# Kernel optimization log

Hardware: AMD Instinct MI355X
Metric: run time of the kernel (lower is better)

The kernel has to match this reference:

```python
import jax, jax.numpy as jnp
import numpy as np

N_WORDS, MAX_CHARS = 32768, 16
WORD_DIM, CHAR_DIM, HIDDEN = 256, 64, 256
VOCAB = 256


def setup_inputs() -> dict:
    key = jax.random.key(0)
    ks = jax.random.split(key, 10)
    char_indices = jax.random.randint(ks[0], (N_WORDS, MAX_CHARS), 0, VOCAB)
    char_lengths = jax.random.randint(ks[1], (N_WORDS,), 1, MAX_CHARS + 1)
    word_emb = jax.random.normal(ks[2], (N_WORDS, WORD_DIM), dtype=jnp.float32)
    s = 0.05
    E_char = jax.random.normal(ks[3], (VOCAB, CHAR_DIM), dtype=jnp.float32) * s
    W_ih = jax.random.normal(ks[4], (4 * HIDDEN, CHAR_DIM), dtype=jnp.float32) * s
    W_hh = jax.random.normal(ks[5], (4 * HIDDEN, HIDDEN), dtype=jnp.float32) * s
    b_ih = jax.random.normal(ks[6], (4 * HIDDEN,), dtype=jnp.float32) * s
    b_hh = jax.random.normal(ks[7], (4 * HIDDEN,), dtype=jnp.float32) * s
    W_lin = jax.random.normal(ks[8], (WORD_DIM, WORD_DIM + HIDDEN), dtype=jnp.float32) * s
    b_lin = jax.random.normal(ks[9], (WORD_DIM,), dtype=jnp.float32) * s
    return dict(char_indices=char_indices, char_lengths=char_lengths,
                word_emb=word_emb, E_char=E_char, W_ih=W_ih, W_hh=W_hh,
                b_ih=b_ih, b_hh=b_hh, W_lin=W_lin, b_lin=b_lin)


def _lstm_last_hidden(x, lengths, W_ih, W_hh, b_ih, b_hh):
    # x: [N, T, E]; returns final hidden h at position length-1 per row.
    N, T, _ = x.shape
    H = W_hh.shape[1]
    x_proj = jnp.einsum('nte,ge->ntg', x, W_ih) + (b_ih + b_hh)  # [N, T, 4H]
    x_proj = jnp.transpose(x_proj, (1, 0, 2))                    # time-major [T, N, 4H]

    def step(carry, inp):
        h, c = carry
        xg, t = inp
        gates = xg + h @ W_hh.T
        i, f, g, o = jnp.split(gates, 4, axis=-1)
        i, f, o = jax.nn.sigmoid(i), jax.nn.sigmoid(f), jax.nn.sigmoid(o)
        g = jnp.tanh(g)
        c_new = f * c + i * g
        h_new = o * jnp.tanh(c_new)
        mask = (t < lengths)[:, None]  # freeze state past each word's length
        h = jnp.where(mask, h_new, h)
        c = jnp.where(mask, c_new, c)
        return (h, c), None

    h0 = jnp.zeros((N, H), dtype=x.dtype)
    c0 = jnp.zeros((N, H), dtype=x.dtype)
    (h, _), _ = jax.lax.scan(step, (h0, c0), (x_proj, jnp.arange(T)))
    return h


def reference(char_indices, char_lengths, word_emb, E_char, W_ih, W_hh,
              b_ih, b_hh, W_lin, b_lin):
    char_embedded = E_char[char_indices]                        # [N, T, E]
    h = _lstm_last_hidden(char_embedded, char_lengths, W_ih, W_hh, b_ih, b_hh)
    combined = jnp.concatenate([word_emb, h], axis=-1)          # [N, WORD+H]
    return jax.nn.relu(combined @ W_lin.T + b_lin)              # [N, WORD]
```

## Files before the change

kernel.cpp:

```cpp
#include <hip/hip_runtime.h>


#define NW 32768

typedef __attribute__((ext_vector_type(8))) short short8;
typedef __attribute__((ext_vector_type(4))) float f32x4;
typedef __attribute__((ext_vector_type(4))) int i32x4;

#define MFMA16(a,b,c) __builtin_amdgcn_mfma_f32_16x16x32_bf16(a,b,c,0,0,0)
#define MFMAI8(a,b,c) __builtin_amdgcn_mfma_i32_16x16x32_i8(a,b,c,0,0,0)

#define O_ORDER 0
#define O_SLEN  131072
#define O_WPK   262144
#define O_USTP  589824
#define O_BIAS  593920
#define O_CHT   598016
#define O_WLIN  614400

__device__ inline unsigned short f2b(float f) {
  unsigned u = __builtin_bit_cast(unsigned, f);
  u = u + 0x7fffu + ((u >> 16) & 1u);
  return (unsigned short)(u >> 16);
}
__device__ inline float fsigm(float x) {
  float e = __builtin_amdgcn_exp2f(-1.44269504f * x);
  return __builtin_amdgcn_rcpf(1.0f + e);
}
__device__ inline float ftanh(float x) {
  float e = __builtin_amdgcn_exp2f(2.88539008f * x);
  return 1.0f - 2.0f * __builtin_amdgcn_rcpf(e + 1.0f);
}

__global__ void k_prep0(const float* __restrict__ wih, const float* __restrict__ whh,
                        const float* __restrict__ bih, const float* __restrict__ bhh,
                        const float* __restrict__ ech, unsigned char* __restrict__ ws) {
  int i = blockIdx.x * 256 + threadIdx.x;
  if (i < 1024) {
    float mx = 0.f;
    for (int k = 0; k < 64; ++k)  mx = fmaxf(mx, fabsf(wih[i * 64 + k]) * 0.25f);
    for (int k = 0; k < 256; ++k) mx = fmaxf(mx, fabsf(whh[i * 256 + k]));
    ((float*)(ws + O_USTP))[i] = mx / (127.f * 127.f);
    ((float*)(ws + O_BIAS))[i] = bih[i] + bhh[i];
    return;
  }
  int j = i - 1024;
  if (j < 16384) {
    float v = 508.f * ech[j];
    int q = (int)__builtin_rintf(v);
    q = q < -127 ? -127 : (q > 127 ? 127 : q);
    ((signed char*)(ws + O_CHT))[j] = (signed char)q;
  }
}

__global__ void k_prep1(const float* __restrict__ wih, const float* __restrict__ whh,
                        const float* __restrict__ wlin, unsigned char* __restrict__ ws) {
  int i = blockIdx.x * 256 + threadIdx.x;
  if (i < 327680) {
    int j = i & 7, lane = (i >> 3) & 63, t2 = i >> 9;
    int nt = t2 & 7, u2 = t2 >> 3;
    int kb = u2 % 10, w = u2 / 10;
    int n = (nt >> 1) * 256 + w * 32 + (nt & 1) * 16 + (lane & 15);
    int k = kb * 32 + (lane >> 4) * 8 + j;
    float v = (k < 64) ? wih[n * 64 + k] * 0.25f : whh[n * 256 + (k - 64)];
    float ustep = ((const float*)(ws + O_USTP))[n] * 127.f;
    float qf = (ustep > 0.f) ? v / ustep : 0.f;
    int q = (int)__builtin_rintf(qf);
    q = q < -127 ? -127 : (q > 127 ? 127 : q);
    ((signed char*)(ws + O_WPK))[i] = (signed char)q;
    return;
  }
  int i2 = i - 327680;
  if (i2 < 131072) {
    int j = i2 & 7, lane = (i2 >> 3) & 63, t3 = i2 >> 9;
    int kf = t3 & 15, nn = t3 >> 4;
    int n = (nn >> 2) * 64 + (nn & 3) * 16 + (lane & 15);
    int k = kf * 32 + (lane >> 4) * 8 + j;
    ((unsigned short*)(ws + O_WLIN))[i2] = f2b(wlin[n * 512 + k]);
  }
}

__global__ void k_sort(const int* __restrict__ lens, unsigned char* __restrict__ ws) {
  __shared__ unsigned hist[16], pos[16];
  int tid = threadIdx.x;
  if (tid < 16) hist[tid] = 0;
  __syncthreads();
  for (int w = tid; w < NW; w += 1024) {
    int l = lens[w]; l = l < 1 ? 1 : (l > 16 ? 16 : l);
    atomicAdd(&hist[l - 1], 1u);
  }
  __syncthreads();
  if (tid == 0) {
    unsigned acc = 0;
    for (int l = 0; l < 16; ++l) { pos[l] = acc; acc += hist[l]; }
  }
  __syncthreads();
  int* order = (int*)(ws + O_ORDER);
  int* slenp = (int*)(ws + O_SLEN);
  for (int w = tid; w < NW; w += 1024) {
    int l = lens[w]; l = l < 1 ? 1 : (l > 16 ? 16 : l);
    unsigned p = atomicAdd(&pos[l - 1], 1u);
    order[p] = w; slenp[p] = l;
  }
}

__global__ __launch_bounds__(512, 2) void k_main(
    const int* __restrict__ cidx, const float* __restrict__ wemb,
    const float* __restrict__ blin, float* __restrict__ outp,
    const unsigned char* __restrict__ ws) {
  extern __shared__ signed char smem[];
  signed char (*WL)[8][8][64][8] = (signed char (*)[8][8][64][8])smem;
  signed char (*Xb)[10][64][8] = (signed char (*)[10][64][8])(smem + 98304);
  signed char (*CT)[64] = (signed char (*)[64])(smem + 98304 + 20480);
  int (*CW)[16] = (int (*)[16])(smem + 98304 + 20480 + 16384);

  const int tid = threadIdx.x, b = blockIdx.x;
  const int w = tid >> 6, lane = tid & 63;
  const int q = lane >> 4, l15 = lane & 15;

  const int* order = (const int*)(ws + O_ORDER);
  const int* slen  = (const int*)(ws + O_SLEN);
  const signed char* wpk = (const signed char*)(ws + O_WPK);
  const float* upt = (const float*)(ws + O_USTP);
  const float* bsg = (const float*)(ws + O_BIAS);
  const unsigned short* wlin = (const unsigned short*)(ws + O_WLIN);

  {
    long* d = (long*)&CT[0][0];
    const long* s = (const long*)(ws + O_CHT);
    #pragma unroll
    for (int ii = 0; ii < 4; ++ii) d[tid + 512 * ii] = s[tid + 512 * ii];
  }
  long wreg[7][8];
  #pragma unroll
  for (int kb = 0; kb < 7; ++kb)
    #pragma unroll
    for (int nt = 0; nt < 8; ++nt)
      wreg[kb][nt] = *(const long*)(wpk + (((w * 10 + kb) * 8 + nt) * 64 + lane) * 8);
  #pragma unroll
  for (int c = 0; c < 24; ++c) {
    int kb = c >> 3, nt = c & 7;
    *(long*)&WL[kb][w][nt][lane][0] =
        *(const long*)(wpk + (((w * 10 + 7 + kb) * 8 + nt) * 64 + lane) * 8);
  }
  float uq[8], bq[8];
  #pragma unroll
  for (int nt = 0; nt < 8; ++nt) {
    int n = (nt >> 1) * 256 + w * 32 + (nt & 1) * 16 + l15;
    uq[nt] = upt[n]; bq[nt] = bsg[n];
  }
  const int mh = w >> 2, nw = w & 3;
  float blv[4];
  #pragma unroll
  for (int nt = 0; nt < 4; ++nt) blv[nt] = blin[nw * 64 + nt * 16 + l15];

  for (int sl = 0; sl < 2; ++sl) {
    const int s = sl ? (511 - b) : b;
    const int base = 64 * s;
    __syncthreads();

    {
      long* p = (long*)&Xb[0][0][0][0];
      #pragma unroll
      for (int ii = 0; ii < 4; ++ii) {
        int idx = tid + 512 * ii;
        int mt = idx >> 9, rem = idx & 511;
        p[mt * 640 + 128 + rem] = 0L;
      }
    }
    if (tid < 256) {
      int m = tid >> 2, part = tid & 3;
      int wid = order[base + m];
      *(i32x4*)&CW[m][part * 4] = *(const i32x4*)(cidx + wid * 16 + part * 4);
    }
    int tmax[4]; unsigned lenpk[4];
    #pragma unroll
    for (int mt = 0; mt < 4; ++mt) {
      int pbm = base + 16 * mt;
      tmax[mt] = slen[pbm + 15];
      unsigned l0 = (unsigned)slen[pbm + q * 4 + 0];
      unsigned l1 = (unsigned)slen[pbm + q * 4 + 1];
      unsigned l2 = (unsigned)slen[pbm + q * 4 + 2];
      unsigned l3 = (unsigned)slen[pbm + q * 4 + 3];
      lenpk[mt] = l0 | (l1 << 8) | (l2 << 16) | (l3 << 24);
    }
    const int Tm = tmax[3];
    __syncthreads();
    {
      int m = tid >> 3, c = tid & 7, kb = c >> 2, kq = c & 3;
      int ch = CW[m][0] & 255;
      *(long*)&Xb[m >> 4][kb][(m & 15) + 16 * kq][0] = *(const long*)&CT[ch][kb * 32 + kq * 8];
    }
    __syncthreads();

    float creg[4][2][4];
    #pragma unroll
    for (int mt = 0; mt < 4; ++mt)
      #pragma unroll
      for (int hs = 0; hs < 2; ++hs)
        #pragma unroll
        for (int r = 0; r < 4; ++r) creg[mt][hs][r] = 0.f;
    unsigned hpack[4][2];

    for (int t = 0; t < Tm; ++t) {
      bool actm[4];
      actm[0] = t < tmax[0]; actm[1] = t < tmax[1];
      actm[2] = t < tmax[2]; actm[3] = true;

      #pragma unroll
      for (int mt = 0; mt < 4; ++mt) {
        if (!actm[mt]) continue;
        i32x4 acc[8];
        #pragma unroll
        for (int nt = 0; nt < 8; ++nt) acc[nt] = (i32x4)0;
        #pragma unroll
        for (int kb = 0; kb < 7; ++kb) {
          long A = *(const long*)&Xb[mt][kb][lane][0];
          #pragma unroll
          for (int nt = 0; nt < 8; ++nt) acc[nt] = MFMAI8(A, wreg[kb][nt], acc[nt]);
        }
        #pragma unroll
        for (int kb = 7; kb < 10; ++kb) {
          long A = *(const long*)&Xb[mt][kb][lane][0];
          #pragma unroll
          for (int nt = 0; nt < 8; ++nt) {
            long Bv = *(const long*)&WL[kb - 7][w][nt][lane][0];
            acc[nt] = MFMAI8(A, Bv, acc[nt]);
          }
        }
        #pragma unroll
        for (int hs = 0; hs < 2; ++hs) {
          unsigned hp = 0;
          #pragma unroll
          for (int r = 0; r < 4; ++r) {
            float gi = (float)acc[0 + hs][r] * uq[0 + hs] + bq[0 + hs];
            float gf = (float)acc[2 + hs][r] * uq[2 + hs] + bq[2 + hs];
            float gg = (float)acc[4 + hs][r] * uq[4 + hs] + bq[4 + hs];
            float go = (float)acc[6 + hs][r] * uq[6 + hs] + bq[6 + hs];
            float si = fsigm(gi), sf = fsigm(gf);
            float sg = ftanh(gg), so = fsigm(go);
            float cold = creg[mt][hs][r];
            float cn = sf * cold + si * sg;
            float hn = so * ftanh(cn);
            int lene = (int)((lenpk[mt] >> (8 * r)) & 255u);
            creg[mt][hs][r] = (t < lene) ? cn : cold;
            int hq = (int)__builtin_rintf(127.f * hn);
            hq = hq < -127 ? -127 : (hq > 127 ? 127 : hq);
            hp |= ((unsigned)hq & 255u) << (8 * r);
          }
          hpack[mt][hs] = hp;
        }
      }
      __syncthreads();

      #pragma unroll
      for (int mt = 0; mt < 4; ++mt) {
        if (!actm[mt]) continue;
        #pragma unroll
        for (int hs = 0; hs < 2; ++hs) {
          int kqp = hs * 2 + (l15 >> 3);
          #pragma unroll
          for (int r = 0; r < 4; ++r) {
            int lene = (int)((lenpk[mt] >> (8 * r)) & 255u);
            if (t < lene)
              Xb[mt][2 + w][(q * 4 + r) + 16 * kqp][l15 & 7] =
                  (signed char)((hpack[mt][hs] >> (8 * r)) & 255u);
          }
        }
      }
      if (t + 1 < Tm) {
        int m = tid >> 3, c = tid & 7, kb = c >> 2, kq = c & 3;
        int ch = CW[m][t + 1] & 255;
        *(long*)&Xb[m >> 4][kb][(m & 15) + 16 * kq][0] = *(const long*)&CT[ch][kb * 32 + kq * 8];
      }
      __syncthreads();
    }

    int widA[2];
    #pragma unroll
    for (int mi = 0; mi < 2; ++mi) widA[mi] = order[base + (2 * mh + mi) * 16 + l15];
    f32x4 fac[2][4];
    #pragma unroll
    for (int mi = 0; mi < 2; ++mi)
      #pragma unroll
      for (int nt = 0; nt < 4; ++nt) fac[mi][nt] = 0.0f;

    #pragma unroll
    for (int kf = 0; kf < 16; ++kf) {
      short8 Bn[4];
      #pragma unroll
      for (int nt = 0; nt < 4; ++nt)
        Bn[nt] = ((const short8*)wlin)[((nw * 4 + nt) * 16 + kf) * 64 + lane];
      short8 Am[2];
      #pragma unroll
      for (int mi = 0; mi < 2; ++mi) {
        if (kf < 8) {
          const f32x4* pa = (const f32x4*)(wemb + widA[mi] * 256 + kf * 32 + q * 8);
          f32x4 f0 = pa[0], f1 = pa[1];
          short8 A;
          A[0] = (short)f2b(f0[0]); A[1] = (short)f2b(f0[1]);
          A[2] = (short)f2b(f0[2]); A[3] = (short)f2b(f0[3]);
          A[4] = (short)f2b(f1[0]); A[5] = (short)f2b(f1[1]);
          A[6] = (short)f2b(f1[2]); A[7] = (short)f2b(f1[3]);
          Am[mi] = A;
        } else {
          long ch = *(const long*)&Xb[2 * mh + mi][kf - 6][lane][0];
          short8 A;
          #pragma unroll
          for (int j = 0; j < 8; ++j) {
            int v = (int)(signed char)((ch >> (8 * j)) & 255);
            A[j] = (short)f2b((float)v * (1.f / 127.f));
          }
          Am[mi] = A;
        }
      }
      #pragma unroll
      for (int mi = 0; mi < 2; ++mi)
        #pragma unroll
        for (int nt = 0; nt < 4; ++nt)
          fac[mi][nt] = MFMA16(Am[mi], Bn[nt], fac[mi][nt]);
    }
    #pragma unroll
    for (int mi = 0; mi < 2; ++mi) {
      #pragma unroll
      for (int r = 0; r < 4; ++r) {
        int wid = order[base + (2 * mh + mi) * 16 + q * 4 + r];
        float* po = outp + wid * 256 + nw * 64 + l15;
        #pragma unroll
        for (int nt = 0; nt < 4; ++nt) {
          float v = fac[mi][nt][r] + blv[nt];
          po[nt * 16] = v > 0.f ? v : 0.f;
        }
      }
    }
  }
}

extern "C" void kernel_launch(void* const* d_in, const int* in_sizes, int n_in,
                              void* d_out, int out_size, void* d_ws, size_t ws_size,
                              hipStream_t stream) {
  const int*   cidx = (const int*)d_in[0];
  const int*   clen = (const int*)d_in[1];
  const float* wemb = (const float*)d_in[2];
  const float* ech  = (const float*)d_in[3];
  const float* wih  = (const float*)d_in[4];
  const float* whh  = (const float*)d_in[5];
  const float* bih  = (const float*)d_in[6];
  const float* bhh  = (const float*)d_in[7];
  const float* wlin = (const float*)d_in[8];
  const float* blin = (const float*)d_in[9];
  float* outp = (float*)d_out;
  unsigned char* ws = (unsigned char*)d_ws;

  k_prep0<<<68, 256, 0, stream>>>(wih, whh, bih, bhh, ech, ws);
  k_prep1<<<1792, 256, 0, stream>>>(wih, whh, wlin, ws);
  k_sort<<<1, 1024, 0, stream>>>(clen, ws);
  k_main<<<256, 512, 139264, stream>>>(cidx, wemb, blin, outp, ws);
}
```

Baseline: 449.7 us.

## Use 1024-thread LSTM blocks with 16x16x64 int8 MFMA and parallel sort

The main kernel moves from 512 to 1024 threads per block, so each wave owns 16 hidden units across all four gates. The recurrent weights now fit entirely in registers using the wider i8 MFMA (K=64), which removes the LDS-resident weight slice. Cell state moves from registers into shared memory. The single-block length sort becomes a per-block histogram in the prep kernel, a prefix pass, and an atomic scatter kernel. The new scatter order is nondeterministic within a length bucket, and the cell state now costs an LDS round trip every step.

```diff
diff --git a/kernel.cpp b/kernel.cpp
--- a/kernel.cpp
+++ b/kernel.cpp
@@ -7,8 +7,8 @@
 typedef __attribute__((ext_vector_type(4))) float f32x4;
 typedef __attribute__((ext_vector_type(4))) int i32x4;
 
-#define MFMA16(a,b,c) __builtin_amdgcn_mfma_f32_16x16x32_bf16(a,b,c,0,0,0)
-#define MFMAI8(a,b,c) __builtin_amdgcn_mfma_i32_16x16x32_i8(a,b,c,0,0,0)
+#define MFMA16(a,b,c)  __builtin_amdgcn_mfma_f32_16x16x32_bf16(a,b,c,0,0,0)
+#define MFMAI64(a,b,c) __builtin_amdgcn_mfma_i32_16x16x64_i8(a,b,c,0,0,0)
 
 #define O_ORDER 0
 #define O_SLEN  131072
@@ -17,6 +17,8 @@
 #define O_BIAS  593920
 #define O_CHT   598016
 #define O_WLIN  614400
+#define O_HP    876544
+#define O_POS   877568
 
 __device__ inline unsigned short f2b(float f) {
   unsigned u = __builtin_bit_cast(unsigned, f);
@@ -32,36 +34,55 @@
   return 1.0f - 2.0f * __builtin_amdgcn_rcpf(e + 1.0f);
 }
 
-__global__ void k_prep0(const float* __restrict__ wih, const float* __restrict__ whh,
+__global__ void k_prepA(const float* __restrict__ wih, const float* __restrict__ whh,
                         const float* __restrict__ bih, const float* __restrict__ bhh,
-                        const float* __restrict__ ech, unsigned char* __restrict__ ws) {
-  int i = blockIdx.x * 256 + threadIdx.x;
-  if (i < 1024) {
-    float mx = 0.f;
-    for (int k = 0; k < 64; ++k)  mx = fmaxf(mx, fabsf(wih[i * 64 + k]) * 0.25f);
-    for (int k = 0; k < 256; ++k) mx = fmaxf(mx, fabsf(whh[i * 256 + k]));
-    ((float*)(ws + O_USTP))[i] = mx / (127.f * 127.f);
-    ((float*)(ws + O_BIAS))[i] = bih[i] + bhh[i];
+                        const float* __restrict__ ech, const int* __restrict__ lens,
+                        unsigned char* __restrict__ ws) {
+  int b = blockIdx.x, tid = threadIdx.x;
+  if (b < 256) {
+    int n = b * 4 + (tid >> 6), lane = tid & 63;
+    float m = fabsf(wih[n * 64 + lane]) * 0.25f;
+    #pragma unroll
+    for (int c = 0; c < 4; ++c) m = fmaxf(m, fabsf(whh[n * 256 + c * 64 + lane]));
+    #pragma unroll
+    for (int off = 32; off; off >>= 1) m = fmaxf(m, __shfl_xor(m, off));
+    if (lane == 0) {
+      ((float*)(ws + O_USTP))[n] = m / 16129.f;
+      ((float*)(ws + O_BIAS))[n] = bih[n] + bhh[n];
+    }
     return;
   }
-  int j = i - 1024;
-  if (j < 16384) {
-    float v = 508.f * ech[j];
-    int q = (int)__builtin_rintf(v);
+  if (b < 320) {
+    int idx = (b - 256) * 256 + tid;
+    int q = (int)__builtin_rintf(508.f * ech[idx]);
     q = q < -127 ? -127 : (q > 127 ? 127 : q);
-    ((signed char*)(ws + O_CHT))[j] = (signed char)q;
-  }
-}
-
-__global__ void k_prep1(const float* __restrict__ wih, const float* __restrict__ whh,
+    ((signed char*)(ws + O_CHT))[idx] = (signed char)q;
+    return;
+  }
+  __shared__ unsigned hist[16];
+  int blk = b - 320;
+  if (tid < 16) hist[tid] = 0;
+  __syncthreads();
+  #pragma unroll
+  for (int i = 0; i < 8; ++i) {
+    int w = blk * 2048 + i * 256 + tid;
+    int l = lens[w]; l = l < 1 ? 1 : (l > 16 ? 16 : l);
+    atomicAdd(&hist[l - 1], 1u);
+  }
+  __syncthreads();
+  if (tid < 16) ((unsigned*)(ws + O_HP))[blk * 16 + tid] = hist[tid];
+}
+
+__global__ void k_prepB(const float* __restrict__ wih, const float* __restrict__ whh,
                         const float* __restrict__ wlin, unsigned char* __restrict__ ws) {
-  int i = blockIdx.x * 256 + threadIdx.x;
-  if (i < 327680) {
-    int j = i & 7, lane = (i >> 3) & 63, t2 = i >> 9;
-    int nt = t2 & 7, u2 = t2 >> 3;
-    int kb = u2 % 10, w = u2 / 10;
-    int n = (nt >> 1) * 256 + w * 32 + (nt & 1) * 16 + (lane & 15);
-    int k = kb * 32 + (lane >> 4) * 8 + j;
+  int b = blockIdx.x, tid = threadIdx.x;
+  int i = b * 256 + tid;
+  if (b < 1280) {
+    int j = i & 15, lane = (i >> 4) & 63, t = i >> 10;
+    int g = t & 3, u = t >> 2;
+    int kb = u % 5, w = u / 5;
+    int n = g * 256 + w * 16 + (lane & 15);
+    int k = kb * 64 + (lane >> 4) * 16 + j;
     float v = (k < 64) ? wih[n * 64 + k] * 0.25f : whh[n * 256 + (k - 64)];
     float ustep = ((const float*)(ws + O_USTP))[n] * 127.f;
     float qf = (ustep > 0.f) ? v / ustep : 0.f;
@@ -70,49 +91,48 @@
     ((signed char*)(ws + O_WPK))[i] = (signed char)q;
     return;
   }
-  int i2 = i - 327680;
-  if (i2 < 131072) {
+  if (b < 1792) {
+    int i2 = i - 327680;
     int j = i2 & 7, lane = (i2 >> 3) & 63, t3 = i2 >> 9;
     int kf = t3 & 15, nn = t3 >> 4;
     int n = (nn >> 2) * 64 + (nn & 3) * 16 + (lane & 15);
     int k = kf * 32 + (lane >> 4) * 8 + j;
     ((unsigned short*)(ws + O_WLIN))[i2] = f2b(wlin[n * 512 + k]);
-  }
-}
-
-__global__ void k_sort(const int* __restrict__ lens, unsigned char* __restrict__ ws) {
-  __shared__ unsigned hist[16], pos[16];
-  int tid = threadIdx.x;
-  if (tid < 16) hist[tid] = 0;
-  __syncthreads();
-  for (int w = tid; w < NW; w += 1024) {
-    int l = lens[w]; l = l < 1 ? 1 : (l > 16 ? 16 : l);
-    atomicAdd(&hist[l - 1], 1u);
-  }
-  __syncthreads();
+    return;
+  }
   if (tid == 0) {
+    const unsigned* hp = (const unsigned*)(ws + O_HP);
+    int* pos = (int*)(ws + O_POS);
     unsigned acc = 0;
-    for (int l = 0; l < 16; ++l) { pos[l] = acc; acc += hist[l]; }
-  }
-  __syncthreads();
-  int* order = (int*)(ws + O_ORDER);
-  int* slenp = (int*)(ws + O_SLEN);
-  for (int w = tid; w < NW; w += 1024) {
-    int l = lens[w]; l = l < 1 ? 1 : (l > 16 ? 16 : l);
-    unsigned p = atomicAdd(&pos[l - 1], 1u);
-    order[p] = w; slenp[p] = l;
-  }
-}
-
-__global__ __launch_bounds__(512, 2) void k_main(
+    for (int l = 0; l < 16; ++l) {
+      unsigned s = 0;
+      for (int blk = 0; blk < 16; ++blk) s += hp[blk * 16 + l];
+      pos[l] = (int)acc; acc += s;
+    }
+  }
+}
+
+__global__ void k_scatter(const int* __restrict__ lens, unsigned char* __restrict__ ws) {
+  int w = blockIdx.x * 256 + threadIdx.x;
+  int l = lens[w]; l = l < 1 ? 1 : (l > 16 ? 16 : l);
+  int p = atomicAdd((int*)(ws + O_POS) + (l - 1), 1);
+  ((int*)(ws + O_ORDER))[p] = w;
+  ((int*)(ws + O_SLEN))[p]  = l;
+}
+
+#define L_XB  65536
+#define L_CT  86016
+#define L_CW  102400
+
+__global__ __launch_bounds__(1024, 4) void k_main(
     const int* __restrict__ cidx, const float* __restrict__ wemb,
     const float* __restrict__ blin, float* __restrict__ outp,
     const unsigned char* __restrict__ ws) {
-  extern __shared__ signed char smem[];
-  signed char (*WL)[8][8][64][8] = (signed char (*)[8][8][64][8])smem;
-  signed char (*Xb)[10][64][8] = (signed char (*)[10][64][8])(smem + 98304);
-  signed char (*CT)[64] = (signed char (*)[64])(smem + 98304 + 20480);
-  int (*CW)[16] = (int (*)[16])(smem + 98304 + 20480 + 16384);
+  extern __shared__ unsigned char smem[];
+  float* CRG = (float*)smem;
+  signed char (*Xb)[5][64][16] = (signed char (*)[5][64][16])(smem + L_XB);
+  signed char (*CT)[64] = (signed char (*)[64])(smem + L_CT);
+  int (*CW)[16] = (int (*)[16])(smem + L_CW);
 
   const int tid = threadIdx.x, b = blockIdx.x;
   const int w = tid >> 6, lane = tid & 63;
@@ -121,35 +141,23 @@
   const int* order = (const int*)(ws + O_ORDER);
   const int* slen  = (const int*)(ws + O_SLEN);
   const signed char* wpk = (const signed char*)(ws + O_WPK);
-  const float* upt = (const float*)(ws + O_USTP);
-  const float* bsg = (const float*)(ws + O_BIAS);
   const unsigned short* wlin = (const unsigned short*)(ws + O_WLIN);
 
-  {
-    long* d = (long*)&CT[0][0];
-    const long* s = (const long*)(ws + O_CHT);
-    #pragma unroll
-    for (int ii = 0; ii < 4; ++ii) d[tid + 512 * ii] = s[tid + 512 * ii];
-  }
-  long wreg[7][8];
+  ((i32x4*)CT)[tid] = ((const i32x4*)(ws + O_CHT))[tid];
+  i32x4 wreg[5][4];
   #pragma unroll
-  for (int kb = 0; kb < 7; ++kb)
-    #pragma unroll
-    for (int nt = 0; nt < 8; ++nt)
-      wreg[kb][nt] = *(const long*)(wpk + (((w * 10 + kb) * 8 + nt) * 64 + lane) * 8);
+  for (int kb = 0; kb < 5; ++kb)
+    #pragma unroll
+    for (int g = 0; g < 4; ++g)
+      wreg[kb][g] = *(const i32x4*)(wpk + (((w * 5 + kb) * 4 + g) * 64 + lane) * 16);
+  float uq[4], bq[4];
   #pragma unroll
-  for (int c = 0; c < 24; ++c) {
-    int kb = c >> 3, nt = c & 7;
-    *(long*)&WL[kb][w][nt][lane][0] =
-        *(const long*)(wpk + (((w * 10 + 7 + kb) * 8 + nt) * 64 + lane) * 8);
-  }
-  float uq[8], bq[8];
-  #pragma unroll
-  for (int nt = 0; nt < 8; ++nt) {
-    int n = (nt >> 1) * 256 + w * 32 + (nt & 1) * 16 + l15;
-    uq[nt] = upt[n]; bq[nt] = bsg[n];
-  }
-  const int mh = w >> 2, nw = w & 3;
+  for (int g = 0; g < 4; ++g) {
+    int n = g * 256 + w * 16 + l15;
+    uq[g] = ((const float*)(ws + O_USTP))[n];
+    bq[g] = ((const float*)(ws + O_BIAS))[n];
+  }
+  const int mt0 = w >> 2, nw = w & 3;
   float blv[4];
   #pragma unroll
   for (int nt = 0; nt < 4; ++nt) blv[nt] = blin[nw * 64 + nt * 16 + l15];
@@ -159,15 +167,10 @@
     const int base = 64 * s;
     __syncthreads();
 
-    {
-      long* p = (long*)&Xb[0][0][0][0];
-      #pragma unroll
-      for (int ii = 0; ii < 4; ++ii) {
-        int idx = tid + 512 * ii;
-        int mt = idx >> 9, rem = idx & 511;
-        p[mt * 640 + 128 + rem] = 0L;
-      }
-    }
+    ((i32x4*)Xb)[tid] = (i32x4)0;
+    if (tid < 256) ((i32x4*)Xb)[1024 + tid] = (i32x4)0;
+    #pragma unroll
+    for (int i = 0; i < 4; ++i) ((i32x4*)CRG)[tid + 1024 * i] = (i32x4)0;
     if (tid < 256) {
       int m = tid >> 2, part = tid & 3;
       int wid = order[base + m];
@@ -186,21 +189,14 @@
     }
     const int Tm = tmax[3];
     __syncthreads();
-    {
-      int m = tid >> 3, c = tid & 7, kb = c >> 2, kq = c & 3;
+    if (tid < 256) {
+      int m = tid >> 2, c = tid & 3;
       int ch = CW[m][0] & 255;
-      *(long*)&Xb[m >> 4][kb][(m & 15) + 16 * kq][0] = *(const long*)&CT[ch][kb * 32 + kq * 8];
+      *(i32x4*)&Xb[m >> 4][0][(m & 15) + 16 * c][0] = *(const i32x4*)&CT[ch][c * 16];
     }
     __syncthreads();
 
-    float creg[4][2][4];
-    #pragma unroll
-    for (int mt = 0; mt < 4; ++mt)
-      #pragma unroll
-      for (int hs = 0; hs < 2; ++hs)
-        #pragma unroll
-        for (int r = 0; r < 4; ++r) creg[mt][hs][r] = 0.f;
-    unsigned hpack[4][2];
+    unsigned hpack[4];
 
     for (int t = 0; t < Tm; ++t) {
       bool actm[4];
@@ -210,46 +206,34 @@
       #pragma unroll
       for (int mt = 0; mt < 4; ++mt) {
         if (!actm[mt]) continue;
-        i32x4 acc[8];
-        #pragma unroll
-        for (int nt = 0; nt < 8; ++nt) acc[nt] = (i32x4)0;
-        #pragma unroll
-        for (int kb = 0; kb < 7; ++kb) {
-          long A = *(const long*)&Xb[mt][kb][lane][0];
+        i32x4 acc[4];
+        #pragma unroll
+        for (int g = 0; g < 4; ++g) acc[g] = (i32x4)0;
+        #pragma unroll
+        for (int kb = 0; kb < 5; ++kb) {
+          i32x4 A = *(const i32x4*)&Xb[mt][kb][lane][0];
           #pragma unroll
-          for (int nt = 0; nt < 8; ++nt) acc[nt] = MFMAI8(A, wreg[kb][nt], acc[nt]);
+          for (int g = 0; g < 4; ++g) acc[g] = MFMAI64(A, wreg[kb][g], acc[g]);
         }
-        #pragma unroll
-        for (int kb = 7; kb < 10; ++kb) {
-          long A = *(const long*)&Xb[mt][kb][lane][0];
-          #pragma unroll
-          for (int nt = 0; nt < 8; ++nt) {
-            long Bv = *(const long*)&WL[kb - 7][w][nt][lane][0];
-            acc[nt] = MFMAI8(A, Bv, acc[nt]);
-          }
+        unsigned hp = 0;
+        #pragma unroll
+        for (int r = 0; r < 4; ++r) {
+          float gi = (float)acc[0][r] * uq[0] + bq[0];
+          float gf = (float)acc[1][r] * uq[1] + bq[1];
+          float gg = (float)acc[2][r] * uq[2] + bq[2];
+          float go = (float)acc[3][r] * uq[3] + bq[3];
+          float si = fsigm(gi), sf = fsigm(gf);
+          float sg = ftanh(gg), so = fsigm(go);
+          float cold = CRG[(mt * 4 + r) * 1024 + tid];
+          float cn = sf * cold + si * sg;
+          float hn = so * ftanh(cn);
+          int lene = (int)((lenpk[mt] >> (8 * r)) & 255u);
+          CRG[(mt * 4 + r) * 1024 + tid] = (t < lene) ? cn : cold;
+          int hq = (int)__builtin_rintf(127.f * hn);
+          hq = hq < -127 ? -127 : (hq > 127 ? 127 : hq);
+          hp |= ((unsigned)hq & 255u) << (8 * r);
         }
-        #pragma unroll
-        for (int hs = 0; hs < 2; ++hs) {
-          unsigned hp = 0;
-          #pragma unroll
-          for (int r = 0; r < 4; ++r) {
-            float gi = (float)acc[0 + hs][r] * uq[0 + hs] + bq[0 + hs];
-            float gf = (float)acc[2 + hs][r] * uq[2 + hs] + bq[2 + hs];
-            float gg = (float)acc[4 + hs][r] * uq[4 + hs] + bq[4 + hs];
-            float go = (float)acc[6 + hs][r] * uq[6 + hs] + bq[6 + hs];
-            float si = fsigm(gi), sf = fsigm(gf);
-            float sg = ftanh(gg), so = fsigm(go);
-            float cold = creg[mt][hs][r];
-            float cn = sf * cold + si * sg;
-            float hn = so * ftanh(cn);
-            int lene = (int)((lenpk[mt] >> (8 * r)) & 255u);
-            creg[mt][hs][r] = (t < lene) ? cn : cold;
-            int hq = (int)__builtin_rintf(127.f * hn);
-            hq = hq < -127 ? -127 : (hq > 127 ? 127 : hq);
-            hp |= ((unsigned)hq & 255u) << (8 * r);
-          }
-          hpack[mt][hs] = hp;
-        }
+        hpack[mt] = hp;
       }
       __syncthreads();
 
@@ -257,33 +241,25 @@
       for (int mt = 0; mt < 4; ++mt) {
         if (!actm[mt]) continue;
         #pragma unroll
-        for (int hs = 0; hs < 2; ++hs) {
-          int kqp = hs * 2 + (l15 >> 3);
-          #pragma unroll
-          for (int r = 0; r < 4; ++r) {
-            int lene = (int)((lenpk[mt] >> (8 * r)) & 255u);
-            if (t < lene)
-              Xb[mt][2 + w][(q * 4 + r) + 16 * kqp][l15 & 7] =
-                  (signed char)((hpack[mt][hs] >> (8 * r)) & 255u);
-          }
+        for (int r = 0; r < 4; ++r) {
+          int lene = (int)((lenpk[mt] >> (8 * r)) & 255u);
+          if (t < lene)
+            Xb[mt][1 + (w >> 2)][(q * 4 + r) + 16 * (w & 3)][l15] =
+                (signed char)((hpack[mt] >> (8 * r)) & 255u);
         }
       }
-      if (t + 1 < Tm) {
-        int m = tid >> 3, c = tid & 7, kb = c >> 2, kq = c & 3;
+      if (t + 1 < Tm && tid < 256) {
+        int m = tid >> 2, c = tid & 3;
         int ch = CW[m][t + 1] & 255;
-        *(long*)&Xb[m >> 4][kb][(m & 15) + 16 * kq][0] = *(const long*)&CT[ch][kb * 32 + kq * 8];
+        *(i32x4*)&Xb[m >> 4][0][(m & 15) + 16 * c][0] = *(const i32x4*)&CT[ch][c * 16];
       }
       __syncthreads();
     }
 
-    int widA[2];
-    #pragma unroll
-    for (int mi = 0; mi < 2; ++mi) widA[mi] = order[base + (2 * mh + mi) * 16 + l15];
-    f32x4 fac[2][4];
-    #pragma unroll
-    for (int mi = 0; mi < 2; ++mi)
-      #pragma unroll
-      for (int nt = 0; nt < 4; ++nt) fac[mi][nt] = 0.0f;
+    int widA = order[base + mt0 * 16 + l15];
+    f32x4 fac[4];
+    #pragma unroll
+    for (int nt = 0; nt < 4; ++nt) fac[nt] = 0.0f;
 
     #pragma unroll
     for (int kf = 0; kf < 16; ++kf) {
@@ -291,46 +267,34 @@
       #pragma unroll
       for (int nt = 0; nt < 4; ++nt)
         Bn[nt] = ((const short8*)wlin)[((nw * 4 + nt) * 16 + kf) * 64 + lane];
-      short8 Am[2];
-      #pragma unroll
-      for (int mi = 0; mi < 2; ++mi) {
-        if (kf < 8) {
-          const f32x4* pa = (const f32x4*)(wemb + widA[mi] * 256 + kf * 32 + q * 8);
-          f32x4 f0 = pa[0], f1 = pa[1];
-          short8 A;
-          A[0] = (short)f2b(f0[0]); A[1] = (short)f2b(f0[1]);
-          A[2] = (short)f2b(f0[2]); A[3] = (short)f2b(f0[3]);
-          A[4] = (short)f2b(f1[0]); A[5] = (short)f2b(f1[1]);
-          A[6] = (short)f2b(f1[2]); A[7] = (short)f2b(f1[3]);
-          Am[mi] = A;
-        } else {
-          long ch = *(const long*)&Xb[2 * mh + mi][kf - 6][lane][0];
-          short8 A;
-          #pragma unroll
-          for (int j = 0; j < 8; ++j) {
-            int v = (int)(signed char)((ch >> (8 * j)) & 255);
-            A[j] = (short)f2b((float)v * (1.f / 127.f));
-          }
-          Am[mi] = A;
+      short8 Am;
+      if (kf < 8) {
+        const f32x4* pa = (const f32x4*)(wemb + widA * 256 + kf * 32 + q * 8);
+        f32x4 f0 = pa[0], f1 = pa[1];
+        Am[0] = (short)f2b(f0[0]); Am[1] = (short)f2b(f0[1]);
+        Am[2] = (short)f2b(f0[2]); Am[3] = (short)f2b(f0[3]);
+        Am[4] = (short)f2b(f1[0]); Am[5] = (short)f2b(f1[1]);
+        Am[6] = (short)f2b(f1[2]); Am[7] = (short)f2b(f1[3]);
+      } else {
+        int K0 = 64 + (kf - 8) * 32 + q * 8;
+        long ch = *(const long*)&Xb[mt0][K0 >> 6][l15 + 16 * ((K0 >> 4) & 3)][K0 & 15];
+        #pragma unroll
+        for (int j = 0; j < 8; ++j) {
+          int v = (int)(signed char)((ch >> (8 * j)) & 255);
+          Am[j] = (short)f2b((float)v * (1.f / 127.f));
         }
       }
       #pragma unroll
-      for (int mi = 0; mi < 2; ++mi)
-        #pragma unroll
-        for (int nt = 0; nt < 4; ++nt)
-          fac[mi][nt] = MFMA16(Am[mi], Bn[nt], fac[mi][nt]);
-    }
-    #pragma unroll
-    for (int mi = 0; mi < 2; ++mi) {
-      #pragma unroll
-      for (int r = 0; r < 4; ++r) {
-        int wid = order[base + (2 * mh + mi) * 16 + q * 4 + r];
-        float* po = outp + wid * 256 + nw * 64 + l15;
-        #pragma unroll
-        for (int nt = 0; nt < 4; ++nt) {
-          float v = fac[mi][nt][r] + blv[nt];
-          po[nt * 16] = v > 0.f ? v : 0.f;
-        }
+      for (int nt = 0; nt < 4; ++nt) fac[nt] = MFMA16(Am, Bn[nt], fac[nt]);
+    }
+    #pragma unroll
+    for (int r = 0; r < 4; ++r) {
+      int wid = order[base + mt0 * 16 + q * 4 + r];
+      float* po = outp + wid * 256 + nw * 64 + l15;
+      #pragma unroll
+      for (int nt = 0; nt < 4; ++nt) {
+        float v = fac[nt][r] + blv[nt];
+        po[nt * 16] = v > 0.f ? v : 0.f;
       }
     }
   }
@@ -352,8 +316,8 @@
   float* outp = (float*)d_out;
   unsigned char* ws = (unsigned char*)d_ws;
 
-  k_prep0<<<68, 256, 0, stream>>>(wih, whh, bih, bhh, ech, ws);
-  k_prep1<<<1792, 256, 0, stream>>>(wih, whh, wlin, ws);
-  k_sort<<<1, 1024, 0, stream>>>(clen, ws);
-  k_main<<<256, 512, 139264, stream>>>(cidx, wemb, blin, outp, ws);
-}
+  k_prepA<<<336, 256, 0, stream>>>(wih, whh, bih, bhh, ech, clen, ws);
+  k_prepB<<<1793, 256, 0, stream>>>(wih, whh, wlin, ws);
+  k_scatter<<<128, 256, 0, stream>>>(clen, ws);
+  k_main<<<256, 1024, 106496, stream>>>(cidx, wemb, blin, outp, ws);
+}
```

After: 571.3 us. +27.0%, slower.

## Merge gate reciprocals, drop per-tile time skipping, parallelize weight-scale prep

Applied to the files above, without the earlier changes.

The LSTM cell math now folds the sigmoid and tanh reciprocals into fewer rcp calls, so i*g and o*tanh(c) each use a single reciprocal of a product, with clamping added to avoid overflow. The per-16-row tile activity check is removed, so every tile runs the MFMA and gate work for all steps up to the block's maximum length. The state is still frozen through per-row length masks. The prep kernel computes per-row max-abs scales with a wave-wide shuffle reduction instead of a serial loop per thread. Removing the skip adds wasted work for short words in sorted blocks, in exchange for fewer transcendental ops and less branching.

```diff
diff --git a/kernel.cpp b/kernel.cpp
--- a/kernel.cpp
+++ b/kernel.cpp
@@ -23,34 +23,28 @@
   u = u + 0x7fffu + ((u >> 16) & 1u);
   return (unsigned short)(u >> 16);
 }
-__device__ inline float fsigm(float x) {
-  float e = __builtin_amdgcn_exp2f(-1.44269504f * x);
-  return __builtin_amdgcn_rcpf(1.0f + e);
-}
-__device__ inline float ftanh(float x) {
-  float e = __builtin_amdgcn_exp2f(2.88539008f * x);
-  return 1.0f - 2.0f * __builtin_amdgcn_rcpf(e + 1.0f);
-}
-
-__global__ void k_prep0(const float* __restrict__ wih, const float* __restrict__ whh,
+
+__global__ void k_prepA(const float* __restrict__ wih, const float* __restrict__ whh,
                         const float* __restrict__ bih, const float* __restrict__ bhh,
                         const float* __restrict__ ech, unsigned char* __restrict__ ws) {
-  int i = blockIdx.x * 256 + threadIdx.x;
-  if (i < 1024) {
-    float mx = 0.f;
-    for (int k = 0; k < 64; ++k)  mx = fmaxf(mx, fabsf(wih[i * 64 + k]) * 0.25f);
-    for (int k = 0; k < 256; ++k) mx = fmaxf(mx, fabsf(whh[i * 256 + k]));
-    ((float*)(ws + O_USTP))[i] = mx / (127.f * 127.f);
-    ((float*)(ws + O_BIAS))[i] = bih[i] + bhh[i];
+  int b = blockIdx.x, tid = threadIdx.x;
+  if (b < 256) {
+    int n = b * 4 + (tid >> 6), lane = tid & 63;
+    float m = fabsf(wih[n * 64 + lane]) * 0.25f;
+    #pragma unroll
+    for (int c = 0; c < 4; ++c) m = fmaxf(m, fabsf(whh[n * 256 + c * 64 + lane]));
+    #pragma unroll
+    for (int off = 32; off; off >>= 1) m = fmaxf(m, __shfl_xor(m, off));
+    if (lane == 0) {
+      ((float*)(ws + O_USTP))[n] = m / 16129.f;
+      ((float*)(ws + O_BIAS))[n] = bih[n] + bhh[n];
+    }
     return;
   }
-  int j = i - 1024;
-  if (j < 16384) {
-    float v = 508.f * ech[j];
-    int q = (int)__builtin_rintf(v);
-    q = q < -127 ? -127 : (q > 127 ? 127 : q);
-    ((signed char*)(ws + O_CHT))[j] = (signed char)q;
-  }
+  int idx = (b - 256) * 256 + tid;
+  int q = (int)__builtin_rintf(508.f * ech[idx]);
+  q = q < -127 ? -127 : (q > 127 ? 127 : q);
+  ((signed char*)(ws + O_CHT))[idx] = (signed char)q;
 }
 
 __global__ void k_prep1(const float* __restrict__ wih, const float* __restrict__ whh,
@@ -71,13 +65,11 @@
     return;
   }
   int i2 = i - 327680;
-  if (i2 < 131072) {
-    int j = i2 & 7, lane = (i2 >> 3) & 63, t3 = i2 >> 9;
-    int kf = t3 & 15, nn = t3 >> 4;
-    int n = (nn >> 2) * 64 + (nn & 3) * 16 + (lane & 15);
-    int k = kf * 32 + (lane >> 4) * 8 + j;
-    ((unsigned short*)(ws + O_WLIN))[i2] = f2b(wlin[n * 512 + k]);
-  }
+  int j = i2 & 7, lane = (i2 >> 3) & 63, t3 = i2 >> 9;
+  int kf = t3 & 15, nn = t3 >> 4;
+  int n = (nn >> 2) * 64 + (nn & 3) * 16 + (lane & 15);
+  int k = kf * 32 + (lane >> 4) * 8 + j;
+  ((unsigned short*)(ws + O_WLIN))[i2] = f2b(wlin[n * 512 + k]);
 }
 
 __global__ void k_sort(const int* __restrict__ lens, unsigned char* __restrict__ ws) {
@@ -173,18 +165,17 @@
       int wid = order[base + m];
       *(i32x4*)&CW[m][part * 4] = *(const i32x4*)(cidx + wid * 16 + part * 4);
     }
-    int tmax[4]; unsigned lenpk[4];
+    unsigned lenpk[4];
     #pragma unroll
     for (int mt = 0; mt < 4; ++mt) {
       int pbm = base + 16 * mt;
-      tmax[mt] = slen[pbm + 15];
       unsigned l0 = (unsigned)slen[pbm + q * 4 + 0];
       unsigned l1 = (unsigned)slen[pbm + q * 4 + 1];
       unsigned l2 = (unsigned)slen[pbm + q * 4 + 2];
       unsigned l3 = (unsigned)slen[pbm + q * 4 + 3];
       lenpk[mt] = l0 | (l1 << 8) | (l2 << 16) | (l3 << 24);
     }
-    const int Tm = tmax[3];
+    const int Tm = slen[base + 63];
     __syncthreads();
     {
       int m = tid >> 3, c = tid & 7, kb = c >> 2, kq = c & 3;
@@ -203,13 +194,8 @@
     unsigned hpack[4][2];
 
     for (int t = 0; t < Tm; ++t) {
-      bool actm[4];
-      actm[0] = t < tmax[0]; actm[1] = t < tmax[1];
-      actm[2] = t < tmax[2]; actm[3] = true;
-
       #pragma unroll
       for (int mt = 0; mt < 4; ++mt) {
-        if (!actm[mt]) continue;
         i32x4 acc[8];
         #pragma unroll
         for (int nt = 0; nt < 8; ++nt) acc[nt] = (i32x4)0;
@@ -237,13 +223,22 @@
             float gf = (float)acc[2 + hs][r] * uq[2 + hs] + bq[2 + hs];
             float gg = (float)acc[4 + hs][r] * uq[4 + hs] + bq[4 + hs];
             float go = (float)acc[6 + hs][r] * uq[6 + hs] + bq[6 + hs];
-            float si = fsigm(gi), sf = fsigm(gf);
-            float sg = ftanh(gg), so = fsigm(go);
+            gi = fminf(30.f, fmaxf(-30.f, gi));
+            gf = fminf(30.f, fmaxf(-30.f, gf));
+            gg = fminf(30.f, fmaxf(-30.f, gg));
+            go = fminf(30.f, fmaxf(-30.f, go));
+            float ei  = __builtin_amdgcn_exp2f(-1.44269504f * gi);
+            float ef  = __builtin_amdgcn_exp2f(-1.44269504f * gf);
+            float eg2 = __builtin_amdgcn_exp2f( 2.88539008f * gg);
+            float eo  = __builtin_amdgcn_exp2f(-1.44269504f * go);
             float cold = creg[mt][hs][r];
-            float cn = sf * cold + si * sg;
-            float hn = so * ftanh(cn);
+            float cn = cold * __builtin_amdgcn_rcpf(1.f + ef) +
+                       (eg2 - 1.f) * __builtin_amdgcn_rcpf((1.f + ei) * (1.f + eg2));
+            float ec = __builtin_amdgcn_exp2f(2.88539008f * cn);
+            float hn = (ec - 1.f) * __builtin_amdgcn_rcpf((1.f + eo) * (ec + 1.f));
             int lene = (int)((lenpk[mt] >> (8 * r)) & 255u);
-            creg[mt][hs][r] = (t < lene) ? cn : cold;
+            bool act = t < lene;
+            creg[mt][hs][r] = act ? cn : cold;
             int hq = (int)__builtin_rintf(127.f * hn);
             hq = hq < -127 ? -127 : (hq > 127 ? 127 : hq);
             hp |= ((unsigned)hq & 255u) << (8 * r);
@@ -255,7 +250,6 @@
 
       #pragma unroll
       for (int mt = 0; mt < 4; ++mt) {
-        if (!actm[mt]) continue;
         #pragma unroll
         for (int hs = 0; hs < 2; ++hs) {
           int kqp = hs * 2 + (l15 >> 3);
@@ -352,7 +346,7 @@
   float* outp = (float*)d_out;
   unsigned char* ws = (unsigned char*)d_ws;
 
-  k_prep0<<<68, 256, 0, stream>>>(wih, whh, bih, bhh, ech, ws);
+  k_prepA<<<320, 256, 0, stream>>>(wih, whh, bih, bhh, ech, ws);
   k_prep1<<<1792, 256, 0, stream>>>(wih, whh, wlin, ws);
   k_sort<<<1, 1024, 0, stream>>>(clen, ws);
   k_main<<<256, 512, 139264, stream>>>(cidx, wemb, blin, outp, ws);
```

Measured after the change: 730.3 us. 62.4% more time.
